# Performance work log

Measured on AMD Instinct MI355X. Metric: run time of the kernel, lower is better.

Reference implementation:

```python
import jax, jax.numpy as jnp
import numpy as np
from jax import lax

PLANES = 256
STRIDE = 1
REMOVED_RATIO = 0.5  # gvar.get_value('r') in original code


def setup_inputs() -> dict:
    key = jax.random.key(0)
    k1, k2 = jax.random.split(key)
    x = jax.random.normal(k1, (32, 256, 56, 56), dtype=jnp.float32)
    w_spt = jax.random.normal(k2, (1, 2, 3, 3), dtype=jnp.float32) * 0.1  # OIHW
    return {"x": x, "w_spt": w_spt}


def reference(x, w_spt):
    # channel pooling: [B,1,H,W] each
    y_max = jnp.max(x, axis=1, keepdims=True)
    y_avg = jnp.mean(x, axis=1, keepdims=True)
    y = jnp.concatenate([y_max, y_avg], axis=1)  # [B,2,H,W]
    # conv3x3(2->1, stride, pad=1, no bias) + sigmoid
    y = lax.conv_general_dilated(
        y, w_spt,
        window_strides=(STRIDE, STRIDE),
        padding=((1, 1), (1, 1)),
        dimension_numbers=("NCHW", "OIHW", "NCHW"),
    )
    y = jax.nn.sigmoid(y)  # [B,1,h,w]
    b, _, h, w = y.shape
    yf = y.reshape(b, h * w)
    # Topk: zero the removed_num smallest-|.| entries per row
    removed_num = int(np.round(h * w * REMOVED_RATIO))
    if removed_num > 0:
        idx = jnp.argsort(jnp.abs(yf), axis=1)[:, :removed_num]  # [b, k]
        rows = jnp.arange(b)[:, None]
        yf = yf.at[rows, idx].set(0.0)
    y = yf.reshape(b, 1, h, w)
    return jnp.broadcast_to(y, (b, PLANES, h, w))
```

## Files before the change

kernel.cpp:

```cpp
#include <hip/hip_runtime.h>
#include <math.h>

#define HW      3136
#define WIDTH   56
#define PADW    58
#define K_REM   1568
#define NBATCH  32
#define NCHAN   256
#define NOWN    13

__global__ __launch_bounds__(256) void pool_kernel(const float* __restrict__ x,
                                                   float* __restrict__ pooled) {
    int p  = blockIdx.x * 256 + threadIdx.x;
    int b  = p / HW;
    int hw = p - b * HW;
    const float* px = x + (size_t)b * NCHAN * HW + hw;

    float mx = px[0];
    float s[8];
#pragma unroll
    for (int j = 0; j < 8; ++j) s[j] = 0.f;

#pragma unroll 16
    for (int c = 0; c < NCHAN; ++c) {
        float v = px[(size_t)c * HW];
        mx = fmaxf(mx, v);
        s[c & 7] += v;
    }
    float t0 = s[0] + s[1], t1 = s[2] + s[3], t2 = s[4] + s[5], t3 = s[6] + s[7];
    float u0 = t0 + t1, u1 = t2 + t3;
    float mean = (u0 + u1) * (1.0f / 256.0f);

    pooled[(size_t)b * 2 * HW + hw]      = mx;
    pooled[(size_t)b * 2 * HW + HW + hw] = mean;
}

__global__ __launch_bounds__(256) void select_kernel(const float* __restrict__ pooled,
                                                     const float* __restrict__ w,
                                                     float* __restrict__ plane) {
    const int b   = blockIdx.x;
    const int tid = threadIdx.x;

    __shared__ float sm0[PADW * PADW];
    __shared__ float sm1[PADW * PADW];
    __shared__ float yvs[HW];
    __shared__ int   wsum[2][4];

    for (int i = tid; i < PADW * PADW; i += 256) { sm0[i] = 0.f; sm1[i] = 0.f; }
    __syncthreads();

    const float* pb = pooled + (size_t)b * 2 * HW;
    for (int i = tid; i < HW; i += 256) {
        int r = i / WIDTH, c = i - r * WIDTH;
        sm0[(r + 1) * PADW + (c + 1)] = pb[i];
        sm1[(r + 1) * PADW + (c + 1)] = pb[HW + i];
    }
    float wreg[18];
#pragma unroll
    for (int j = 0; j < 18; ++j) wreg[j] = w[j];
    __syncthreads();

    float    val[NOWN];
    unsigned bits[NOWN];
#pragma unroll
    for (int t = 0; t < NOWN; ++t) {
        int i = tid + 256 * t;
        if (i < HW) {
            int r = i / WIDTH, c = i - r * WIDTH;
            float acc = 0.f;
#pragma unroll
            for (int kr = 0; kr < 3; ++kr)
#pragma unroll
                for (int kc = 0; kc < 3; ++kc) {
                    acc += wreg[kr * 3 + kc]     * sm0[(r + kr) * PADW + (c + kc)];
                    acc += wreg[9 + kr * 3 + kc] * sm1[(r + kr) * PADW + (c + kc)];
                }
            float v = 1.0f / (1.0f + expf(-acc));
            val[t]  = v;
            bits[t] = __float_as_uint(v);
            yvs[i]  = v;
        } else {
            val[t]  = 0.f;
            bits[t] = 0x7FFFFFFFu;
        }
    }
    __syncthreads();

    const int wid  = tid >> 6;
    const int lane = tid & 63;
    const int r    = K_REM - 1;

    unsigned prefix = 0u;
    for (int bit = 29; bit >= 0; --bit) {
        unsigned cand = prefix | (1u << bit);
        int lc = 0;
#pragma unroll
        for (int t = 0; t < NOWN; ++t) lc += (bits[t] < cand) ? 1 : 0;
#pragma unroll
        for (int off = 32; off >= 1; off >>= 1) lc += __shfl_xor(lc, off);
        int par = bit & 1;
        if (lane == 0) wsum[par][wid] = lc;
        __syncthreads();
        int c = wsum[par][0] + wsum[par][1] + wsum[par][2] + wsum[par][3];
        if (c <= r) prefix = cand;
    }
    const unsigned T = prefix;

    {
        int lc = 0;
#pragma unroll
        for (int t = 0; t < NOWN; ++t) {
            lc += (bits[t] < T)  ? 1 : 0;
            lc += (bits[t] == T) ? (1 << 16) : 0;
        }
#pragma unroll
        for (int off = 32; off >= 1; off >>= 1) lc += __shfl_xor(lc, off);
        if (lane == 0) wsum[0][wid] = lc;
        __syncthreads();
    }
    int packed = wsum[0][0] + wsum[0][1] + wsum[0][2] + wsum[0][3];
    int cLess  = packed & 0xFFFF;
    int ce     = packed >> 16;
    int rfin   = r - cLess;

    float* pl = plane + (size_t)b * HW;
#pragma unroll
    for (int t = 0; t < NOWN; ++t) {
        int i = tid + 256 * t;
        if (i >= HW) break;
        float v = val[t];
        unsigned bt = bits[t];
        if (bt < T) {
            v = 0.f;
        } else if (bt == T) {
            if (ce == 1) {
                v = 0.f;
            } else {
                int cnt = 0;
                for (int j = 0; j < i; ++j)
                    cnt += (__float_as_uint(yvs[j]) == T) ? 1 : 0;
                if (cnt <= rfin) v = 0.f;
            }
        }
        pl[i] = v;
    }
}

__global__ __launch_bounds__(256) void bcast_kernel(const float* __restrict__ plane,
                                                    float4* __restrict__ out) {
    int i   = blockIdx.x * 256 + threadIdx.x;
    int hw4 = i % 784;
    int bc  = i / 784;
    int b   = bc >> 8;
    out[i] = ((const float4*)plane)[b * 784 + hw4];
}

extern "C" void kernel_launch(void* const* d_in, const int* in_sizes, int n_in,
                              void* d_out, int out_size, void* d_ws, size_t ws_size,
                              hipStream_t stream) {
    const float* x = (const float*)d_in[0];
    const float* w = (const float*)d_in[1];
    float* out     = (float*)d_out;

    float* pooled = (float*)d_ws;
    float* plane  = pooled + (size_t)NBATCH * 2 * HW;

    pool_kernel  <<<392,   256, 0, stream>>>(x, pooled);
    select_kernel<<<NBATCH,256, 0, stream>>>(pooled, w, plane);
    bcast_kernel <<<25088, 256, 0, stream>>>(plane, (float4*)out);
}
```

Measured before the change: 202.3 us.

## Split channel reduction across eight waves per pixel tile in pool kernel

```diff
diff --git a/kernel.cpp b/kernel.cpp
--- a/kernel.cpp
+++ b/kernel.cpp
@@ -9,30 +9,48 @@
 #define NCHAN   256
 #define NOWN    13
 
-__global__ __launch_bounds__(256) void pool_kernel(const float* __restrict__ x,
+__global__ __launch_bounds__(512) void pool_kernel(const float* __restrict__ x,
                                                    float* __restrict__ pooled) {
-    int p  = blockIdx.x * 256 + threadIdx.x;
-    int b  = p / HW;
-    int hw = p - b * HW;
+    __shared__ float smax[8][64];
+    __shared__ float ssum[8][64];
+
+    const int tid  = threadIdx.x;
+    const int lane = tid & 63;
+    const int wv   = tid >> 6;
+    const int blk  = blockIdx.x;
+    const int b    = blk / 49;
+    const int hw   = (blk - b * 49) * 64 + lane;
+
     const float* px = x + (size_t)b * NCHAN * HW + hw;
 
-    float mx = px[0];
-    float s[8];
-#pragma unroll
-    for (int j = 0; j < 8; ++j) s[j] = 0.f;
+    float mxl = px[(size_t)wv * HW];
+    float sl  = 0.f;
+#pragma unroll 8
+    for (int k = 0; k < 32; ++k) {
+        float v = px[(size_t)(wv + 8 * k) * HW];
+        mxl = fmaxf(mxl, v);
+        sl += v;
+    }
+    smax[wv][lane] = mxl;
+    ssum[wv][lane] = sl;
+    __syncthreads();
 
-#pragma unroll 16
-    for (int c = 0; c < NCHAN; ++c) {
-        float v = px[(size_t)c * HW];
-        mx = fmaxf(mx, v);
-        s[c & 7] += v;
+    if (wv == 0) {
+        float m0 = fmaxf(smax[0][lane], smax[1][lane]);
+        float m1 = fmaxf(smax[2][lane], smax[3][lane]);
+        float m2 = fmaxf(smax[4][lane], smax[5][lane]);
+        float m3 = fmaxf(smax[6][lane], smax[7][lane]);
+        float m  = fmaxf(fmaxf(m0, m1), fmaxf(m2, m3));
+        float t0 = ssum[0][lane] + ssum[1][lane];
+        float t1 = ssum[2][lane] + ssum[3][lane];
+        float t2 = ssum[4][lane] + ssum[5][lane];
+        float t3 = ssum[6][lane] + ssum[7][lane];
+        float u0 = t0 + t1, u1 = t2 + t3;
+        float mean = (u0 + u1) * (1.0f / 256.0f);
+
+        pooled[(size_t)b * 2 * HW + hw]      = m;
+        pooled[(size_t)b * 2 * HW + HW + hw] = mean;
     }
-    float t0 = s[0] + s[1], t1 = s[2] + s[3], t2 = s[4] + s[5], t3 = s[6] + s[7];
-    float u0 = t0 + t1, u1 = t2 + t3;
-    float mean = (u0 + u1) * (1.0f / 256.0f);
-
-    pooled[(size_t)b * 2 * HW + hw]      = mx;
-    pooled[(size_t)b * 2 * HW + HW + hw] = mean;
 }
 
 __global__ __launch_bounds__(256) void select_kernel(const float* __restrict__ pooled,
@@ -165,7 +183,7 @@
     float* pooled = (float*)d_ws;
     float* plane  = pooled + (size_t)NBATCH * 2 * HW;
 
-    pool_kernel  <<<392,   256, 0, stream>>>(x, pooled);
+    pool_kernel  <<<1568,  512, 0, stream>>>(x, pooled);
     select_kernel<<<NBATCH,256, 0, stream>>>(pooled, w, plane);
     bcast_kernel <<<25088, 256, 0, stream>>>(plane, (float4*)out);
 }
```

After: 201.6 us. Within noise of the previous version (-0.4%).
